# Kernel optimization log

Measured on AMD Instinct MI355X. Metric: run time of the kernel, lower is better.

## Reference

```python
import jax, jax.numpy as jnp
import numpy as np

SMOOTH = 0.5  # self.smooth from __init__

def setup_inputs() -> dict:
    key = jax.random.key(0)
    k1, k2, k3, k4, k5, k6 = jax.random.split(key, 6)
    N, E, F_IN, F_OUT = 100000, 3200000, 128, 128
    x = jax.random.normal(k1, (N, F_IN), dtype=jnp.float32)
    adj_rows = jax.random.randint(k2, (E,), 0, N, dtype=jnp.int32)
    adj_cols = jax.random.randint(k3, (E,), 0, N, dtype=jnp.int32)
    adj_vals = jax.random.uniform(k4, (E,), dtype=jnp.float32)
    stdv = 1.0 / np.sqrt(F_OUT)
    weight = jax.random.uniform(k5, (F_IN, F_OUT), dtype=jnp.float32, minval=-stdv, maxval=stdv)
    bias = jax.random.uniform(k6, (F_OUT,), dtype=jnp.float32, minval=-stdv, maxval=stdv)
    return {"x": x, "adj_rows": adj_rows, "adj_cols": adj_cols,
            "adj_vals": adj_vals, "weight": weight, "bias": bias}

def reference(x, adj_rows, adj_cols, adj_vals, weight, bias):
    # support = X @ W  (dense GEMM)
    support = x @ weight  # [N, F_out]
    n = x.shape[0]
    # adj @ support via edge-list gather + segment scatter-add
    gathered = support[adj_cols] * adj_vals[:, None]  # [E, F_out]
    agg = jax.ops.segment_sum(gathered, adj_rows, num_segments=n)  # [N, F_out]
    # ((I + smooth*adj) / (1 + smooth)) @ support + bias
    out = (support + SMOOTH * agg) / (1.0 + SMOOTH) + bias
    return out
```

## Files before the change

kernel.cpp:

```cpp
#include <hip/hip_runtime.h>
#include <hip/hip_fp16.h>

#define F 128
#define BM 64

#define SB_ROWS 256
#define SB_SHIFT 8
#define NBUCK_MAX 512
#define CAPS 9216
#define BIN_BLOCKS 512

#define LSTR 136

typedef _Float16 half8_t __attribute__((ext_vector_type(8)));
typedef float f32x4 __attribute__((ext_vector_type(4)));

__device__ inline __half2 h2of(unsigned u) {
    union { unsigned u; __half2 h; } x; x.u = u; return x.h;
}

__global__ __launch_bounds__(256) void gemm_kernel(
    const float* __restrict__ X, const float* __restrict__ W,
    _Float16* __restrict__ suph, int N)
{
    __shared__ _Float16 Wt[F * LSTR];
    __shared__ _Float16 Xh[BM * LSTR];

    const int t    = threadIdx.x;
    const int row0 = blockIdx.x * BM;

    for (int i = t; i < F * F; i += 256) {
        int k = i >> 7, c = i & 127;
        Wt[c * LSTR + k] = (_Float16)W[i];
    }
    for (int i = t; i < BM * (F / 4); i += 256) {
        int r = i >> 5, k4 = i & 31;
        int grow = row0 + r;
        float4 xv = make_float4(0.f, 0.f, 0.f, 0.f);
        if (grow < N) xv = ((const float4*)(X + (size_t)grow * F))[k4];
        _Float16* xp = &Xh[r * LSTR + k4 * 4];
        xp[0] = (_Float16)xv.x; xp[1] = (_Float16)xv.y;
        xp[2] = (_Float16)xv.z; xp[3] = (_Float16)xv.w;
    }
    __syncthreads();

    const int wv = t >> 6, lane = t & 63;
    const int fr = lane & 15, fq = lane >> 4;

    const _Float16* xa = Xh + (wv * 16 + fr) * LSTR + fq * 8;
    half8_t a0 = *(const half8_t*)(xa);
    half8_t a1 = *(const half8_t*)(xa + 32);
    half8_t a2 = *(const half8_t*)(xa + 64);
    half8_t a3 = *(const half8_t*)(xa + 96);

    #pragma unroll
    for (int tc = 0; tc < 8; ++tc) {
        const _Float16* wb = Wt + (tc * 16 + fr) * LSTR + fq * 8;
        f32x4 acc = {0.f, 0.f, 0.f, 0.f};
        acc = __builtin_amdgcn_mfma_f32_16x16x32_f16(a0, *(const half8_t*)(wb),      acc, 0, 0, 0);
        acc = __builtin_amdgcn_mfma_f32_16x16x32_f16(a1, *(const half8_t*)(wb + 32), acc, 0, 0, 0);
        acc = __builtin_amdgcn_mfma_f32_16x16x32_f16(a2, *(const half8_t*)(wb + 64), acc, 0, 0, 0);
        acc = __builtin_amdgcn_mfma_f32_16x16x32_f16(a3, *(const half8_t*)(wb + 96), acc, 0, 0, 0);

        const int col   = tc * 16 + fr;
        const int rbase = row0 + wv * 16 + fq * 4;
        #pragma unroll
        for (int r = 0; r < 4; ++r) {
            int row = rbase + r;
            if (row < N) suph[(size_t)row * F + col] = (_Float16)acc[r];
        }
    }
}

__global__ __launch_bounds__(256) void bin_kernel(
    const int* __restrict__ rows, const int* __restrict__ cols,
    const float* __restrict__ vals, int* __restrict__ cursor,
    int2* __restrict__ csr, int E, int nbuck)
{
    __shared__ int hist[NBUCK_MAX];
    __shared__ int base[NBUCK_MAX];

    const int t = threadIdx.x;
    int chunk = ((E + BIN_BLOCKS - 1) / BIN_BLOCKS + 3) & ~3;
    const int beg = blockIdx.x * chunk;
    const int end = min(beg + chunk, E);
    if (beg >= E) return;

    for (int b = t; b < nbuck; b += 256) hist[b] = 0;
    __syncthreads();

    int i = beg + t * 4;
    for (; i + 3 < end; i += 1024) {
        int4 r = *(const int4*)(rows + i);
        atomicAdd(&hist[r.x >> SB_SHIFT], 1);
        atomicAdd(&hist[r.y >> SB_SHIFT], 1);
        atomicAdd(&hist[r.z >> SB_SHIFT], 1);
        atomicAdd(&hist[r.w >> SB_SHIFT], 1);
    }
    for (; i < end; ++i) atomicAdd(&hist[rows[i] >> SB_SHIFT], 1);
    __syncthreads();

    for (int b = t; b < nbuck; b += 256) {
        int c = hist[b];
        base[b] = c ? atomicAdd(&cursor[b], c) : 0;
        hist[b] = 0;
    }
    __syncthreads();

    i = beg + t * 4;
    for (; i + 3 < end; i += 1024) {
        int4 r = *(const int4*)(rows + i);
        int4 c = *(const int4*)(cols + i);
        float4 v = *(const float4*)(vals + i);
        int rr[4] = {r.x, r.y, r.z, r.w};
        int cc[4] = {c.x, c.y, c.z, c.w};
        float vv[4] = {v.x, v.y, v.z, v.w};
        #pragma unroll
        for (int k = 0; k < 4; ++k) {
            int b  = rr[k] >> SB_SHIFT;
            int rl = rr[k] & (SB_ROWS - 1);
            int pos = base[b] + atomicAdd(&hist[b], 1);
            if (pos < CAPS)
                csr[(size_t)b * CAPS + pos] =
                    make_int2(cc[k] | (rl << 17), __float_as_int(vv[k]));
        }
    }
    for (; i < end; ++i) {
        int b  = rows[i] >> SB_SHIFT;
        int rl = rows[i] & (SB_ROWS - 1);
        int pos = base[b] + atomicAdd(&hist[b], 1);
        if (pos < CAPS)
            csr[(size_t)b * CAPS + pos] =
                make_int2(cols[i] | (rl << 17), __float_as_int(vals[i]));
    }
}

__global__ __launch_bounds__(512) void sortb_kernel(
    const int* __restrict__ cursor, int2* __restrict__ csr,
    int* __restrict__ offsB, int* __restrict__ offsE, int N)
{
    __shared__ int h[SB_ROWS];
    __shared__ int sc[SB_ROWS];
    __shared__ int lc[SB_ROWS];
    __shared__ int wsum[4];
    __shared__ int2 st[CAPS];

    const int b = blockIdx.x;
    const int t = threadIdx.x;
    const int cnt = min(cursor[b], CAPS);
    int2* reg = csr + (size_t)b * CAPS;

    if (t < SB_ROWS) { h[t] = 0; lc[t] = 0; }
    __syncthreads();

    for (int i = t; i < cnt; i += 512)
        atomicAdd(&h[((unsigned)reg[i].x) >> 17], 1);
    __syncthreads();

    int hv = 0, inc = 0;
    const int lane = t & 63, w = t >> 6;
    if (t < SB_ROWS) {
        hv = h[t];
        inc = hv;
        #pragma unroll
        for (int d = 1; d < 64; d <<= 1) {
            int u = __shfl_up(inc, d, 64);
            if (lane >= d) inc += u;
        }
        if (lane == 63) wsum[w] = inc;
    }
    __syncthreads();
    if (t < SB_ROWS) {
        int wbase = 0;
        for (int ww = 0; ww < w; ++ww) wbase += wsum[ww];
        int ex = inc - hv + wbase;
        sc[t] = ex;
        int row = b * SB_ROWS + t;
        if (row < N) {
            int gbase = b * CAPS;
            offsB[row] = gbase + ex;
            offsE[row] = gbase + ex + hv;
        }
    }
    __syncthreads();

    for (int i = t; i < cnt; i += 512) {
        int2 e = reg[i];
        int rl = ((unsigned)e.x) >> 17;
        int pos = sc[rl] + atomicAdd(&lc[rl], 1);
        st[pos] = make_int2(e.x & 0x1FFFF, e.y);
    }
    __syncthreads();

    for (int i = t; i < cnt; i += 512) reg[i] = st[i];
}

__global__ __launch_bounds__(256) void agg_kernel(
    const int* __restrict__ offsB, const int* __restrict__ offsE,
    const int2* __restrict__ csr, const __half* __restrict__ sup,
    const float* __restrict__ bias, float* __restrict__ out, int N)
{
    int wid  = (int)((blockIdx.x * 256 + threadIdx.x) >> 6);
    if (wid >= N) return;
    int lane = threadIdx.x & 63;
    int g  = lane >> 4;
    int sl = lane & 15;

    const int beg = offsB[wid];
    const int end = offsE[wid];
    const int len = end - beg;
    const int q   = (len + 3) >> 2;
    const int gb  = beg + g * q;
    const int ge  = min(gb + q, end);

    float acc[8];
    #pragma unroll
    for (int i = 0; i < 8; ++i) acc[i] = 0.f;

    int j = gb;
    for (; j + 3 < ge; j += 4) {
        int2 cv0 = csr[j];
        int2 cv1 = csr[j + 1];
        int2 cv2 = csr[j + 2];
        int2 cv3 = csr[j + 3];
        const uint4 s0 = *(const uint4*)(sup + (size_t)cv0.x * F + sl * 8);
        const uint4 s1 = *(const uint4*)(sup + (size_t)cv1.x * F + sl * 8);
        const uint4 s2 = *(const uint4*)(sup + (size_t)cv2.x * F + sl * 8);
        const uint4 s3 = *(const uint4*)(sup + (size_t)cv3.x * F + sl * 8);
        __half2 v0 = __float2half2_rn(__int_as_float(cv0.y));
        __half2 v1 = __float2half2_rn(__int_as_float(cv1.y));
        __half2 v2 = __float2half2_rn(__int_as_float(cv2.y));
        __half2 v3 = __float2half2_rn(__int_as_float(cv3.y));

        __half2 p0 = __hmul2(h2of(s0.x), v0);
        __half2 p1 = __hmul2(h2of(s0.y), v0);
        __half2 p2 = __hmul2(h2of(s0.z), v0);
        __half2 p3 = __hmul2(h2of(s0.w), v0);
        p0 = __hfma2(h2of(s1.x), v1, p0);
        p1 = __hfma2(h2of(s1.y), v1, p1);
        p2 = __hfma2(h2of(s1.z), v1, p2);
        p3 = __hfma2(h2of(s1.w), v1, p3);
        p0 = __hfma2(h2of(s2.x), v2, p0);
        p1 = __hfma2(h2of(s2.y), v2, p1);
        p2 = __hfma2(h2of(s2.z), v2, p2);
        p3 = __hfma2(h2of(s2.w), v2, p3);
        p0 = __hfma2(h2of(s3.x), v3, p0);
        p1 = __hfma2(h2of(s3.y), v3, p1);
        p2 = __hfma2(h2of(s3.z), v3, p2);
        p3 = __hfma2(h2of(s3.w), v3, p3);

        float2 f;
        f = __half22float2(p0); acc[0] += f.x; acc[1] += f.y;
        f = __half22float2(p1); acc[2] += f.x; acc[3] += f.y;
        f = __half22float2(p2); acc[4] += f.x; acc[5] += f.y;
        f = __half22float2(p3); acc[6] += f.x; acc[7] += f.y;
    }
    for (; j < ge; ++j) {
        int2 cv = csr[j];
        const uint4 s = *(const uint4*)(sup + (size_t)cv.x * F + sl * 8);
        __half2 v = __float2half2_rn(__int_as_float(cv.y));
        float2 f;
        f = __half22float2(__hmul2(h2of(s.x), v)); acc[0] += f.x; acc[1] += f.y;
        f = __half22float2(__hmul2(h2of(s.y), v)); acc[2] += f.x; acc[3] += f.y;
        f = __half22float2(__hmul2(h2of(s.z), v)); acc[4] += f.x; acc[5] += f.y;
        f = __half22float2(__hmul2(h2of(s.w), v)); acc[6] += f.x; acc[7] += f.y;
    }

    #pragma unroll
    for (int i = 0; i < 8; ++i) {
        acc[i] += __shfl_xor(acc[i], 16, 64);
        acc[i] += __shfl_xor(acc[i], 32, 64);
    }

    if (g == 0) {
        const uint4 s = *(const uint4*)(sup + (size_t)wid * F + sl * 8);
        float4 b0 = *(const float4*)(bias + sl * 8);
        float4 b1 = *(const float4*)(bias + sl * 8 + 4);
        const float inv = 1.0f / 1.5f, third = 1.0f / 3.0f;
        float2 sA = __half22float2(h2of(s.x));
        float2 sB = __half22float2(h2of(s.y));
        float2 sC = __half22float2(h2of(s.z));
        float2 sD = __half22float2(h2of(s.w));
        float4 o0, o1;
        o0.x = sA.x * inv + acc[0] * third + b0.x;
        o0.y = sA.y * inv + acc[1] * third + b0.y;
        o0.z = sB.x * inv + acc[2] * third + b0.z;
        o0.w = sB.y * inv + acc[3] * third + b0.w;
        o1.x = sC.x * inv + acc[4] * third + b1.x;
        o1.y = sC.y * inv + acc[5] * third + b1.y;
        o1.z = sD.x * inv + acc[6] * third + b1.z;
        o1.w = sD.y * inv + acc[7] * third + b1.w;
        float* op = out + (size_t)wid * F + sl * 8;
        *(float4*)(op)     = o0;
        *(float4*)(op + 4) = o1;
    }
}

extern "C" void kernel_launch(void* const* d_in, const int* in_sizes, int n_in,
                              void* d_out, int out_size, void* d_ws, size_t ws_size,
                              hipStream_t stream) {
    const float* x        = (const float*)d_in[0];
    const int*   adj_rows = (const int*)  d_in[1];
    const int*   adj_cols = (const int*)  d_in[2];
    const float* adj_vals = (const float*)d_in[3];
    const float* weight   = (const float*)d_in[4];
    const float* bias     = (const float*)d_in[5];

    const int N = in_sizes[0] / F;
    const int E = in_sizes[1];
    const int nbuck = (N + SB_ROWS - 1) / SB_ROWS;

    float* out = (float*)d_out;
    char*  ws  = (char*)d_ws;

    auto align = [](size_t v) { return (v + 255) & ~(size_t)255; };
    size_t off_sup    = 0;
    size_t sz_sup     = align((size_t)N * F * sizeof(_Float16));
    size_t off_csr    = off_sup + sz_sup;
    size_t sz_csr     = align((size_t)nbuck * CAPS * sizeof(int2));
    size_t off_offsB  = off_csr + sz_csr;
    size_t sz_offsB   = align((size_t)N * sizeof(int));
    size_t off_offsE  = off_offsB + sz_offsB;
    size_t sz_offsE   = align((size_t)N * sizeof(int));
    size_t off_cursor = off_offsE + sz_offsE;

    _Float16* suph = (_Float16*)(ws + off_sup);
    int2* csr    = (int2*)(ws + off_csr);
    int*  offsB  = (int*) (ws + off_offsB);
    int*  offsE  = (int*) (ws + off_offsE);
    int*  cursor = (int*) (ws + off_cursor);

    hipMemsetAsync(cursor, 0, (size_t)nbuck * sizeof(int), stream);

    gemm_kernel<<<(N + BM - 1) / BM, 256, 0, stream>>>(x, weight, suph, N);

    bin_kernel<<<BIN_BLOCKS, 256, 0, stream>>>(
        adj_rows, adj_cols, adj_vals, cursor, csr, E, nbuck);

    sortb_kernel<<<nbuck, 512, 0, stream>>>(cursor, csr, offsB, offsE, N);

    agg_kernel<<<(N + 3) / 4, 256, 0, stream>>>(
        offsB, offsE, csr, (const __half*)suph, bias, out, N);
}
```

Before: 204.6 us.

## Sort bucket edges by row and column group, keeping edges in registers

The per-bucket sort kernel now keys each edge by its local row plus a 3-bit column group, so edges within a row come out grouped by column range. The intent is better cache locality for the support gathers in the aggregation kernel. Edges are loaded once into registers (18 per thread) instead of being re-read from global memory across passes, and the separate histogram and counter arrays are merged into one scanned array. The bucket capacity is lowered so the staging buffer fits shared memory, which raises the risk of dropping edges in overfull buckets.

New measurement: 201.5 us. No clear change (-1.6%).

```diff
diff --git a/kernel.cpp b/kernel.cpp
--- a/kernel.cpp
+++ b/kernel.cpp
@@ -7,8 +7,11 @@
 #define SB_ROWS 256
 #define SB_SHIFT 8
 #define NBUCK_MAX 512
-#define CAPS 9216
+#define CAPS 8960
+#define KREG 18
 #define BIN_BLOCKS 512
+#define NKEY 2048
+#define COLG_SHIFT 14
 
 #define LSTR 136
 
@@ -139,10 +142,8 @@
     const int* __restrict__ cursor, int2* __restrict__ csr,
     int* __restrict__ offsB, int* __restrict__ offsE, int N)
 {
-    __shared__ int h[SB_ROWS];
-    __shared__ int sc[SB_ROWS];
-    __shared__ int lc[SB_ROWS];
-    __shared__ int wsum[4];
+    __shared__ int sc[NKEY];
+    __shared__ int wsum[8];
     __shared__ int2 st[CAPS];
 
     const int b = blockIdx.x;
@@ -150,45 +151,67 @@
     const int cnt = min(cursor[b], CAPS);
     int2* reg = csr + (size_t)b * CAPS;
 
-    if (t < SB_ROWS) { h[t] = 0; lc[t] = 0; }
-    __syncthreads();
-
-    for (int i = t; i < cnt; i += 512)
-        atomicAdd(&h[((unsigned)reg[i].x) >> 17], 1);
-    __syncthreads();
-
-    int hv = 0, inc = 0;
+    int2 e[KREG];
+    #pragma unroll
+    for (int k = 0; k < KREG; ++k) {
+        int idx = t + k * 512;
+        e[k] = (idx < cnt) ? reg[idx] : make_int2(-1, 0);
+    }
+
+    for (int i = t; i < NKEY; i += 512) sc[i] = 0;
+    __syncthreads();
+
+    #pragma unroll
+    for (int k = 0; k < KREG; ++k) {
+        if (e[k].x >= 0) {
+            unsigned p = (unsigned)e[k].x;
+            int key = (int)(((p >> 17) << 3) | ((p >> COLG_SHIFT) & 7));
+            atomicAdd(&sc[key], 1);
+        }
+    }
+    __syncthreads();
+
+    int c0 = sc[t * 4], c1 = sc[t * 4 + 1], c2 = sc[t * 4 + 2], c3 = sc[t * 4 + 3];
+    int s = c0 + c1 + c2 + c3;
+    int inc = s;
     const int lane = t & 63, w = t >> 6;
+    #pragma unroll
+    for (int d = 1; d < 64; d <<= 1) {
+        int u = __shfl_up(inc, d, 64);
+        if (lane >= d) inc += u;
+    }
+    if (lane == 63) wsum[w] = inc;
+    __syncthreads();
+    int wbase = 0;
+    #pragma unroll
+    for (int ww = 0; ww < 8; ++ww) if (ww < w) wbase += wsum[ww];
+    int run = inc - s + wbase;
+    sc[t * 4]     = run; run += c0;
+    sc[t * 4 + 1] = run; run += c1;
+    sc[t * 4 + 2] = run; run += c2;
+    sc[t * 4 + 3] = run; run += c3;
+    __syncthreads();
+
     if (t < SB_ROWS) {
-        hv = h[t];
-        inc = hv;
-        #pragma unroll
-        for (int d = 1; d < 64; d <<= 1) {
-            int u = __shfl_up(inc, d, 64);
-            if (lane >= d) inc += u;
-        }
-        if (lane == 63) wsum[w] = inc;
-    }
-    __syncthreads();
-    if (t < SB_ROWS) {
-        int wbase = 0;
-        for (int ww = 0; ww < w; ++ww) wbase += wsum[ww];
-        int ex = inc - hv + wbase;
-        sc[t] = ex;
         int row = b * SB_ROWS + t;
         if (row < N) {
             int gbase = b * CAPS;
-            offsB[row] = gbase + ex;
-            offsE[row] = gbase + ex + hv;
-        }
-    }
-    __syncthreads();
-
-    for (int i = t; i < cnt; i += 512) {
-        int2 e = reg[i];
-        int rl = ((unsigned)e.x) >> 17;
-        int pos = sc[rl] + atomicAdd(&lc[rl], 1);
-        st[pos] = make_int2(e.x & 0x1FFFF, e.y);
+            int x0 = sc[t * 8];
+            int x1 = (t == SB_ROWS - 1) ? cnt : sc[t * 8 + 8];
+            offsB[row] = gbase + x0;
+            offsE[row] = gbase + x1;
+        }
+    }
+    __syncthreads();
+
+    #pragma unroll
+    for (int k = 0; k < KREG; ++k) {
+        if (e[k].x >= 0) {
+            unsigned p = (unsigned)e[k].x;
+            int key = (int)(((p >> 17) << 3) | ((p >> COLG_SHIFT) & 7));
+            int pos = atomicAdd(&sc[key], 1);
+            st[pos] = make_int2(e[k].x & 0x1FFFF, e[k].y);
+        }
     }
     __syncthreads();
 
```
